# Performance work log

Hardware: AMD Instinct MI355X
Metric: run time of the kernel (lower is better)

Reference implementation:

```python
import jax, jax.numpy as jnp
import numpy as np

B, N, H, HD = 2, 2048, 16, 64
F = H * HD  # feats = 1024
SQRT_D = float(F) ** 0.5  # module uses sqrt(feats), not sqrt(head_dim)
EPS = 1e-5


def layernorm(x, g, b):
    # LayerNorm over last dim (head_dim), shared gamma/beta across heads
    m = jnp.mean(x, axis=-1, keepdims=True)
    v = jnp.mean(jnp.square(x - m), axis=-1, keepdims=True)
    return (x - m) / jnp.sqrt(v + EPS) * g + b


def setup_inputs() -> dict:
    key = jax.random.key(0)
    ks = jax.random.split(key, 14)
    s = 0.02
    return {
        "x": jax.random.normal(ks[0], (B, N, F), dtype=jnp.float32),
        "ln1_g": jnp.ones((HD,), jnp.float32),
        "ln1_b": jnp.zeros((HD,), jnp.float32),
        "ln2_g": jnp.ones((HD,), jnp.float32),
        "ln2_b": jnp.zeros((HD,), jnp.float32),
        # stacked per-head weights: [H, in, out]
        "wq": jax.random.normal(ks[1], (H, HD, HD), jnp.float32) * s,
        "bq": jnp.zeros((H, HD), jnp.float32),
        "wk": jax.random.normal(ks[2], (H, HD, HD), jnp.float32) * s,
        "bk": jnp.zeros((H, HD), jnp.float32),
        "wv": jax.random.normal(ks[3], (H, HD, HD), jnp.float32) * s,
        "bv": jnp.zeros((H, HD), jnp.float32),
        "wo": jax.random.normal(ks[4], (H, HD, HD), jnp.float32) * s,
        "bo": jnp.zeros((H, HD), jnp.float32),
        "w1": jax.random.normal(ks[5], (H, HD, 4 * HD), jnp.float32) * s,
        "b1": jnp.zeros((H, 4 * HD), jnp.float32),
        "w2": jax.random.normal(ks[6], (H, 4 * HD, HD), jnp.float32) * s,
        "b2": jnp.zeros((H, HD), jnp.float32),
        # Method 0 merge Linear(feats, feats): y = x @ wm + bm
        "wm": jax.random.normal(ks[7], (F, F), jnp.float32) * s,
        "bm": jnp.zeros((F,), jnp.float32),
    }


def reference(x, ln1_g, ln1_b, ln2_g, ln2_b, wq, bq, wk, bk, wv, bv, wo, bo,
              w1, b1, w2, b2, wm, bm):
    b, n, f = x.shape
    x4 = x.reshape(b, n, H, HD)  # [b, n, h, hd]

    # --- Multi-head self attention (per-head linears batched over h) ---
    h1 = layernorm(x4, ln1_g, ln1_b)
    q = jnp.einsum("bnhf,hfg->bnhg", h1, wq) + bq
    k = jnp.einsum("bnhf,hfg->bnhg", h1, wk) + bk
    v = jnp.einsum("bnhf,hfg->bnhg", h1, wv) + bv
    qh = jnp.swapaxes(q, 1, 2)  # [b, h, n, hd]
    kh = jnp.swapaxes(k, 1, 2)
    vh = jnp.swapaxes(v, 1, 2)
    score = jax.nn.softmax(jnp.einsum("bhif,bhjf->bhij", qh, kh) / SQRT_D, axis=-1)
    attn = jnp.einsum("bhij,bhjf->bihf", score, vh)  # [b, n, h, hd]
    attn = jnp.einsum("bnhf,hfg->bnhg", attn, wo) + bo
    out = attn + x4

    # --- Per-head FFN (GELU after BOTH linears, as in source; dropout=0) ---
    h2 = layernorm(out, ln2_g, ln2_b)
    t = jax.nn.gelu(jnp.einsum("bnhf,hfg->bnhg", h2, w1) + b1, approximate=False)
    t = jax.nn.gelu(jnp.einsum("bnhg,hgf->bnhf", t, w2) + b2, approximate=False)
    out = t + out

    # --- Method 0 merge ---
    out = out.reshape(b, n, f)
    out = out @ wm + bm
    return out
```

## Files before the change

### kernel.cpp

```cpp
#include <hip/hip_runtime.h>
#include <hip/hip_bf16.h>
#include <math.h>

#define TOKS 4096
#define NSEQ 2048
#define NH 16
#define DH 64
#define FD 1024

typedef __bf16 bf16_t;
typedef bf16_t bf16x4 __attribute__((ext_vector_type(4)));
typedef bf16_t bf16x8 __attribute__((ext_vector_type(8)));
typedef float f32x4 __attribute__((ext_vector_type(4)));

#define GLL16(gsrc, ldst)                                                        \
    __builtin_amdgcn_global_load_lds(                                            \
        (const __attribute__((address_space(1))) void*)(const void*)(gsrc),      \
        (__attribute__((address_space(3))) void*)(void*)(ldst), 16, 0, 0)

__device__ __forceinline__ float geluf(float x) {
    return 0.5f * x * (1.0f + erff(x * 0.70710678118654752f));
}

__device__ __forceinline__ float fexp2(float x) {
    int i = (int)__builtin_fmaf(x, 8388608.0f, 1065063216.0f);
    return __int_as_float(i);
}

__device__ __forceinline__ int lds_sw(int row, int d) {
    return row * 64 + ((((d >> 3) ^ (row & 7)) & 7) << 3) + (d & 7);
}

__device__ __forceinline__ int vperm(int j) {
    return (j & 32) | ((j & 12) << 1) | ((j & 16) >> 2) | (j & 3);
}

__global__ __launch_bounds__(256) void k_prep(
    const float* __restrict__ wm, const float* __restrict__ w1, const float* __restrict__ w2,
    const float* __restrict__ wq, const float* __restrict__ wk,
    const float* __restrict__ wv, const float* __restrict__ wo,
    bf16_t* __restrict__ wt, bf16_t* __restrict__ w1t, bf16_t* __restrict__ w2t,
    bf16_t* __restrict__ wqt, bf16_t* __restrict__ wkt,
    bf16_t* __restrict__ wvt, bf16_t* __restrict__ wot)
{
    __shared__ bf16_t t[64 * 65];
    const int b = blockIdx.x;
    const int tid = threadIdx.x;
    if (b < 256) {
        const int k0 = (b & 15) * 64, n0 = (b >> 4) * 64;
        #pragma unroll
        for (int it = 0; it < 16; it++) {
            int idx = it * 256 + tid;
            int kk = idx >> 6, nn = idx & 63;
            t[nn * 65 + kk] = (bf16_t)wm[(size_t)(k0 + kk) * FD + n0 + nn];
        }
        __syncthreads();
        #pragma unroll
        for (int it = 0; it < 16; it++) {
            int idx = it * 256 + tid;
            int nn = idx >> 6, kk = idx & 63;
            wt[(size_t)(n0 + nn) * FD + k0 + kk] = t[nn * 65 + kk];
        }
    } else if (b < 320) {
        const int lb = b - 256;
        const int h = lb >> 2, n0 = (lb & 3) * 64;
        const float* src = w1 + (size_t)h * 64 * 256;
        #pragma unroll
        for (int it = 0; it < 16; it++) {
            int idx = it * 256 + tid;
            int kk = idx >> 6, nn = idx & 63;
            t[nn * 65 + kk] = (bf16_t)src[kk * 256 + n0 + nn];
        }
        __syncthreads();
        bf16_t* dst = w1t + (size_t)h * 16384;
        #pragma unroll
        for (int it = 0; it < 16; it++) {
            int idx = it * 256 + tid;
            int nn = idx >> 6, kk = idx & 63;
            int row = n0 + nn;
            dst[row * 64 + ((((kk >> 3) ^ (row & 7)) & 7) << 3) + (kk & 7)] = t[nn * 65 + kk];
        }
    } else if (b < 384) {
        const int lb = b - 320;
        const int h = lb >> 2, k0 = (lb & 3) * 64;
        const float* src = w2 + (size_t)h * 256 * 64;
        #pragma unroll
        for (int it = 0; it < 16; it++) {
            int idx = it * 256 + tid;
            int kk = idx >> 6, nn = idx & 63;
            t[nn * 65 + kk] = (bf16_t)src[(k0 + kk) * 64 + nn];
        }
        __syncthreads();
        bf16_t* dst = w2t + (size_t)h * 16384;
        #pragma unroll
        for (int it = 0; it < 16; it++) {
            int idx = it * 256 + tid;
            int nn = idx >> 6, kk = idx & 63;
            int c = k0 + vperm(kk);
            int chunk = c >> 3;
            int chunkp = (chunk & 24) | ((chunk ^ nn) & 7);
            dst[nn * 256 + (chunkp << 3) + (c & 7)] = t[nn * 65 + kk];
        }
    } else {
        const int h = b - 384;
        const float* srcs[4] = {wq + h * 4096, wk + h * 4096, wv + h * 4096, wo + h * 4096};
        bf16_t* dsts[4] = {wqt + h * 4096, wkt + h * 4096, wvt + h * 4096, wot + h * 4096};
        #pragma unroll
        for (int m = 0; m < 4; m++) {
            __syncthreads();
            #pragma unroll
            for (int it = 0; it < 16; it++) {
                int idx = it * 256 + tid;
                int ff = idx >> 6, gg = idx & 63;
                t[gg * 65 + ff] = (bf16_t)srcs[m][ff * 64 + gg];
            }
            __syncthreads();
            #pragma unroll
            for (int it = 0; it < 16; it++) {
                int idx = it * 256 + tid;
                int gg = idx >> 6, ff = idx & 63;
                if (m == 3)
                    dsts[m][gg * 64 + ((((ff >> 3) ^ (gg & 7)) & 7) << 3) + (ff & 7)] =
                        t[gg * 65 + ff];
                else
                    dsts[m][gg * 64 + ff] = t[gg * 65 + ff];
            }
        }
    }
}

__global__ __launch_bounds__(256) void k_ln1_qkv(
    const float* __restrict__ x, const float* __restrict__ g1, const float* __restrict__ be1,
    const bf16_t* __restrict__ wqt, const float* __restrict__ bq,
    const bf16_t* __restrict__ wkt, const float* __restrict__ bk,
    const bf16_t* __restrict__ wvt, const float* __restrict__ bv,
    bf16_t* __restrict__ q, bf16_t* __restrict__ k, bf16_t* __restrict__ vt)
{
    __shared__ __align__(16) bf16_t h1s[64 * 64];
    __shared__ __align__(16) bf16_t vts[64 * 72];
    const int h  = blockIdx.y;
    const int t0 = blockIdx.x * 64;
    const int tid = threadIdx.x;

    {
        const int i = tid >> 2, s = tid & 3;
        const float* xr = x + (size_t)(t0 + i) * FD + h * DH + s * 16;
        float vals[16];
        #pragma unroll
        for (int r = 0; r < 4; r++) {
            float4 tmp = *(const float4*)(xr + r * 4);
            vals[r*4+0]=tmp.x; vals[r*4+1]=tmp.y; vals[r*4+2]=tmp.z; vals[r*4+3]=tmp.w;
        }
        float sm = 0.f;
        #pragma unroll
        for (int r = 0; r < 16; r++) sm += vals[r];
        sm += __shfl_xor(sm, 1); sm += __shfl_xor(sm, 2);
        const float mean = sm * (1.0f / 64.0f);
        float vr = 0.f;
        #pragma unroll
        for (int r = 0; r < 16; r++) { float d = vals[r] - mean; vr += d * d; }
        vr += __shfl_xor(vr, 1); vr += __shfl_xor(vr, 2);
        const float rstd = rsqrtf(vr * (1.0f / 64.0f) + 1e-5f);
        bf16x8 o0, o1;
        #pragma unroll
        for (int r = 0; r < 8; r++) {
            int d0 = s * 16 + r, d1 = s * 16 + 8 + r;
            o0[r] = (bf16_t)((vals[r]     - mean) * rstd * g1[d0] + be1[d0]);
            o1[r] = (bf16_t)((vals[8 + r] - mean) * rstd * g1[d1] + be1[d1]);
        }
        *(bf16x8*)&h1s[i * 64 + (((s * 2 + 0) ^ (i & 7)) << 3)] = o0;
        *(bf16x8*)&h1s[i * 64 + (((s * 2 + 1) ^ (i & 7)) << 3)] = o1;
    }
    __syncthreads();

    const int wid = tid >> 6, lane = tid & 63;
    const int g = lane >> 4, c0 = lane & 15;
    const int arow = wid * 16 + c0;

    bf16x8 af0 = *(const bf16x8*)&h1s[arow * 64 + (((g    ) ^ (arow & 7)) << 3)];
    bf16x8 af1 = *(const bf16x8*)&h1s[arow * 64 + (((4 + g) ^ (arow & 7)) << 3)];

    const bf16_t* wqh = wqt + h * 4096;
    const bf16_t* wkh = wkt + h * 4096;
    const bf16_t* wvh = wvt + h * 4096;
    f32x4 aq[4], ak[4], av[4];
    #pragma unroll
    for (int ni = 0; ni < 4; ni++) {
        aq[ni] = (f32x4){0.f, 0.f, 0.f, 0.f};
        ak[ni] = (f32x4){0.f, 0.f, 0.f, 0.f};
        av[ni] = (f32x4){0.f, 0.f, 0.f, 0.f};
    }
    #pragma unroll
    for (int ni = 0; ni < 4; ni++) {
        const int col = ni * 16 + c0;
        bf16x8 b0, b1;
        b0 = *(const bf16x8*)(wqh + col * 64 + g * 8);
        b1 = *(const bf16x8*)(wqh + col * 64 + g * 8 + 32);
        aq[ni] = __builtin_amdgcn_mfma_f32_16x16x32_bf16(af0, b0, aq[ni], 0, 0, 0);
        aq[ni] = __builtin_amdgcn_mfma_f32_16x16x32_bf16(af1, b1, aq[ni], 0, 0, 0);
        b0 = *(const bf16x8*)(wkh + col * 64 + g * 8);
        b1 = *(const bf16x8*)(wkh + col * 64 + g * 8 + 32);
        ak[ni] = __builtin_amdgcn_mfma_f32_16x16x32_bf16(af0, b0, ak[ni], 0, 0, 0);
        ak[ni] = __builtin_amdgcn_mfma_f32_16x16x32_bf16(af1, b1, ak[ni], 0, 0, 0);
        b0 = *(const bf16x8*)(wvh + col * 64 + g * 8);
        b1 = *(const bf16x8*)(wvh + col * 64 + g * 8 + 32);
        av[ni] = __builtin_amdgcn_mfma_f32_16x16x32_bf16(af0, b0, av[ni], 0, 0, 0);
        av[ni] = __builtin_amdgcn_mfma_f32_16x16x32_bf16(af1, b1, av[ni], 0, 0, 0);
    }

    const int rowb = wid * 16 + g * 4;
    const int b = t0 >> 11, n0 = t0 & (NSEQ - 1);
    const size_t qkbase = ((size_t)(b * NH + h) * NSEQ + n0) * DH;

    #pragma unroll
    for (int ni = 0; ni < 4; ni++) {
        const int col = ni * 16 + c0;
        const float bb = bv[h * 64 + col];
        #pragma unroll
        for (int r = 0; r < 4; r++) {
            int i = rowb + r;
            vts[col * 72 + vperm(i)] = (bf16_t)(av[ni][r] + bb);
        }
    }
    __syncthreads();

    #pragma unroll
    for (int ni = 0; ni < 4; ni++) {
        const int col = ni * 16 + c0;
        const float bb = bq[h * 64 + col];
        #pragma unroll
        for (int r = 0; r < 4; r++)
            h1s[lds_sw(rowb + r, col)] = (bf16_t)((aq[ni][r] + bb) * 0.045084220f);
    }
    __syncthreads();
    {
        const int row = tid >> 2, cp = (tid & 3) * 2;
        *(bf16x8*)(q + qkbase + row * DH + cp * 8) =
            *(const bf16x8*)&h1s[row * 64 + ((cp ^ (row & 7)) << 3)];
        *(bf16x8*)(q + qkbase + row * DH + (cp + 1) * 8) =
            *(const bf16x8*)&h1s[row * 64 + (((cp + 1) ^ (row & 7)) << 3)];
        const int d = tid >> 2, c16 = tid & 3;
        size_t vbase = ((size_t)(b * NH + h) * DH + d) * NSEQ + n0 + c16 * 16;
        *(bf16x8*)(vt + vbase)     = *(const bf16x8*)&vts[d * 72 + c16 * 16];
        *(bf16x8*)(vt + vbase + 8) = *(const bf16x8*)&vts[d * 72 + c16 * 16 + 8];
    }
    __syncthreads();

    #pragma unroll
    for (int ni = 0; ni < 4; ni++) {
        const int col = ni * 16 + c0;
        const float bb = bk[h * 64 + col];
        #pragma unroll
        for (int r = 0; r < 4; r++)
            h1s[lds_sw(rowb + r, col)] = (bf16_t)(ak[ni][r] + bb);
    }
    __syncthreads();
    {
        const int row = tid >> 2, cp = (tid & 3) * 2;
        *(bf16x8*)(k + qkbase + row * DH + cp * 8) =
            *(const bf16x8*)&h1s[row * 64 + ((cp ^ (row & 7)) << 3)];
        *(bf16x8*)(k + qkbase + row * DH + (cp + 1) * 8) =
            *(const bf16x8*)&h1s[row * 64 + (((cp + 1) ^ (row & 7)) << 3)];
    }
}

__global__ __launch_bounds__(256, 4) void k_attn(
    const bf16_t* __restrict__ qg, const bf16_t* __restrict__ kg,
    const bf16_t* __restrict__ vt, bf16_t* __restrict__ attnb)
{
    __shared__ __align__(16) bf16_t Ks[2][4096];
    __shared__ __align__(16) bf16_t Vs[2][4096];

    const int bx = blockIdx.x;
    const int bh = ((bx & 7) << 2) | ((bx >> 3) & 3);
    const int qb = blockIdx.y;
    const int tid = threadIdx.x;
    const int wid = tid >> 6, lane = tid & 63;
    const int g = lane >> 4, c0 = lane & 15;
    const int prow = wid * 16 + c0;

    bf16x8 aqf[2];
    {
        const int qrow = qb * 64 + prow;
        const bf16_t* qp = qg + ((size_t)bh * NSEQ + qrow) * DH + g * 8;
        aqf[0] = *(const bf16x8*)qp;
        aqf[1] = *(const bf16x8*)(qp + 32);
    }
    bf16x8 ones;
    #pragma unroll
    for (int e = 0; e < 8; e++) ones[e] = (bf16_t)1.0f;

    int soff[4][2];
    #pragma unroll
    for (int cb = 0; cb < 4; cb++)
        #pragma unroll
        for (int kb = 0; kb < 2; kb++) {
            int row = cb * 16 + c0;
            soff[cb][kb] = row * 64 + (((g + (kb << 2)) ^ (row & 7)) << 3);
        }

    const bf16_t* kbase = kg + (size_t)bh * NSEQ * DH;
    const bf16_t* vbase = vt + (size_t)bh * DH * NSEQ;
    const int gA = wid * 2, gB = gA + 1;
    const int lcA = gA * 64 + lane, lcB = gB * 64 + lane;
    const int rowA = lcA >> 3, ccA = (lcA & 7) ^ (rowA & 7);
    const int rowB = lcB >> 3, ccB = (lcB & 7) ^ (rowB & 7);
    const bf16_t* kpA = kbase + rowA * DH + ccA * 8;
    const bf16_t* kpB = kbase + rowB * DH + ccB * 8;
    const bf16_t* vpA = vbase + (size_t)rowA * NSEQ + ccA * 8;
    const bf16_t* vpB = vbase + (size_t)rowB * NSEQ + ccB * 8;

    GLL16(kpA, (char*)&Ks[0][0] + (gA << 10));
    GLL16(kpB, (char*)&Ks[0][0] + (gB << 10));
    GLL16(vpA, (char*)&Vs[0][0] + (gA << 10));
    GLL16(vpB, (char*)&Vs[0][0] + (gB << 10));
    kpA += 64 * DH; kpB += 64 * DH; vpA += 64; vpB += 64;

    f32x4 O[4];
    #pragma unroll
    for (int cb = 0; cb < 4; cb++) O[cb] = (f32x4){0.f, 0.f, 0.f, 0.f};
    f32x4 l_acc = (f32x4){0.f, 0.f, 0.f, 0.f};

    auto tile = [&](const bf16_t* Kc, const bf16_t* Vc,
                    bf16_t* Kn, bf16_t* Vn, bool pref) {
        __syncthreads();
        if (pref) {
            GLL16(kpA, (char*)Kn + (gA << 10));
            GLL16(kpB, (char*)Kn + (gB << 10));
            GLL16(vpA, (char*)Vn + (gA << 10));
            GLL16(vpB, (char*)Vn + (gB << 10));
            kpA += 64 * DH; kpB += 64 * DH; vpA += 64; vpB += 64;
        }

        f32x4 S[4];
        #pragma unroll
        for (int cb = 0; cb < 4; cb++) {
            f32x4 acc = (f32x4){0.f, 0.f, 0.f, 0.f};
            acc = __builtin_amdgcn_mfma_f32_16x16x32_bf16(
                *(const bf16x8*)&Kc[soff[cb][0]], aqf[0], acc, 0, 0, 0);
            acc = __builtin_amdgcn_mfma_f32_16x16x32_bf16(
                *(const bf16x8*)&Kc[soff[cb][1]], aqf[1], acc, 0, 0, 0);
            S[cb] = acc;
        }

        bf16x8 pa0, pa1;
        #pragma unroll
        for (int cb = 0; cb < 2; cb++)
            #pragma unroll
            for (int r = 0; r < 4; r++)
                pa0[cb * 4 + r] = (bf16_t)fexp2(S[cb][r]);
        #pragma unroll
        for (int cb = 0; cb < 2; cb++)
            #pragma unroll
            for (int r = 0; r < 4; r++)
                pa1[cb * 4 + r] = (bf16_t)fexp2(S[2 + cb][r]);

        l_acc = __builtin_amdgcn_mfma_f32_16x16x32_bf16(ones, pa0, l_acc, 0, 0, 0);
        l_acc = __builtin_amdgcn_mfma_f32_16x16x32_bf16(ones, pa1, l_acc, 0, 0, 0);

        #pragma unroll
        for (int cb = 0; cb < 4; cb++) {
            f32x4 acc = O[cb];
            acc = __builtin_amdgcn_mfma_f32_16x16x32_bf16(
                *(const bf16x8*)&Vc[soff[cb][0]], pa0, acc, 0, 0, 0);
            acc = __builtin_amdgcn_mfma_f32_16x16x32_bf16(
                *(const bf16x8*)&Vc[soff[cb][1]], pa1, acc, 0, 0, 0);
            O[cb] = acc;
        }
    };

    #pragma unroll 1
    for (int kt2 = 0; kt2 < 16; kt2++) {
        tile(Ks[0], Vs[0], Ks[1], Vs[1], true);
        tile(Ks[1], Vs[1], Ks[0], Vs[0], kt2 < 15);
    }

    __syncthreads();
    const float inv = 1.0f / l_acc[0];
    bf16_t* Tb = Ks[0];
    #pragma unroll
    for (int cb = 0; cb < 4; cb++)
        #pragma unroll
        for (int r = 0; r < 4; r++) {
            int d = cb * 16 + g * 4 + r;
            Tb[lds_sw(prow, d)] = (bf16_t)(O[cb][r] * inv);
        }
    __syncthreads();
    {
        const int row = tid >> 2, cp = (tid & 3) * 2;
        size_t gbase = ((size_t)bh * NSEQ + qb * 64 + row) * DH;
        *(bf16x8*)(attnb + gbase + cp * 8) =
            *(const bf16x8*)&Tb[row * 64 + ((cp ^ (row & 7)) << 3)];
        *(bf16x8*)(attnb + gbase + (cp + 1) * 8) =
            *(const bf16x8*)&Tb[row * 64 + (((cp + 1) ^ (row & 7)) << 3)];
    }
}

__global__ __launch_bounds__(1024) void k_pffn(
    const bf16_t* __restrict__ attnb, const bf16_t* __restrict__ wot,
    const float* __restrict__ bo, const float* __restrict__ x,
    const float* __restrict__ g2, const float* __restrict__ be2,
    const bf16_t* __restrict__ w1t, const float* __restrict__ b1,
    const bf16_t* __restrict__ w2t, const float* __restrict__ b2,
    bf16_t* __restrict__ outp)
{
    __shared__ __align__(16) bf16_t wos[4096];
    __shared__ __align__(16) bf16_t w1s[16384];
    __shared__ __align__(16) bf16_t w2s[16384];
    __shared__ __align__(16) bf16_t h2s[256 * 64];
    const int h  = blockIdx.y;
    const int t0 = blockIdx.x * 256;
    const int tid = threadIdx.x;
    const int wid = tid >> 6, lane = tid & 63;
    const int g = lane >> 4, c0 = lane & 15;
    const int b = t0 >> 11, n0 = t0 & (NSEQ - 1);
    const int tok = t0 + wid * 16 + c0;

    {
        const bf16_t* s0 = wot + h * 4096;
        const bf16_t* s1 = w1t + (size_t)h * 16384;
        const bf16_t* s2 = w2t + (size_t)h * 16384;
        if (wid < 8)
            GLL16(s0 + wid * 512 + lane * 8, (char*)wos + (wid << 10));
        #pragma unroll
        for (int i = 0; i < 2; i++) {
            int grp = wid * 2 + i;
            GLL16(s1 + grp * 512 + lane * 8, (char*)w1s + (grp << 10));
            GLL16(s2 + grp * 512 + lane * 8, (char*)w2s + (grp << 10));
        }
        __syncthreads();
    }

    const bf16_t* ah = attnb + ((size_t)(b * NH + h) * NSEQ + n0) * DH;
    bf16x8 paf0 = *(const bf16x8*)(ah + (wid * 16 + c0) * DH + g * 8);
    bf16x8 paf1 = *(const bf16x8*)(ah + (wid * 16 + c0) * DH + g * 8 + 32);
    float o1[4][4];
    #pragma unroll
    for (int ni = 0; ni < 4; ni++) {
        f32x4 acc = (f32x4){0.f, 0.f, 0.f, 0.f};
        const int orow = ni * 16 + c0;
        bf16x8 b0  = *(const bf16x8*)&wos[orow * 64 + (((g    ) ^ (orow & 7)) << 3)];
        bf16x8 b1f = *(const bf16x8*)&wos[orow * 64 + (((4 + g) ^ (orow & 7)) << 3)];
        acc = __builtin_amdgcn_mfma_f32_16x16x32_bf16(b0, paf0, acc, 0, 0, 0);
        acc = __builtin_amdgcn_mfma_f32_16x16x32_bf16(b1f, paf1, acc, 0, 0, 0);
        const float4 bo4 = *(const float4*)(bo + h * DH + ni * 16 + g * 4);
        const float4 xr4 = *(const float4*)(x + (size_t)tok * FD + h * DH + ni * 16 + g * 4);
        o1[ni][0] = acc[0] + bo4.x + xr4.x;
        o1[ni][1] = acc[1] + bo4.y + xr4.y;
        o1[ni][2] = acc[2] + bo4.z + xr4.z;
        o1[ni][3] = acc[3] + bo4.w + xr4.w;
    }

    float s = 0.f;
    #pragma unroll
    for (int ni = 0; ni < 4; ni++)
        #pragma unroll
        for (int r = 0; r < 4; r++) s += o1[ni][r];
    s += __shfl_xor(s, 16);
    s += __shfl_xor(s, 32);
    const float mean = s * (1.0f / 64.0f);
    float v = 0.f;
    #pragma unroll
    for (int ni = 0; ni < 4; ni++)
        #pragma unroll
        for (int r = 0; r < 4; r++) { float d = o1[ni][r] - mean; v += d * d; }
    v += __shfl_xor(v, 16);
    v += __shfl_xor(v, 32);
    const float rstd = rsqrtf(v * (1.0f / 64.0f) + 1e-5f);

    const int R = wid * 16 + c0;
    #pragma unroll
    for (int ni = 0; ni < 4; ni++) {
        const float4 g24 = *(const float4*)(g2 + ni * 16 + g * 4);
        const float4 be4 = *(const float4*)(be2 + ni * 16 + g * 4);
        bf16x4 hw;
        hw[0] = (bf16_t)((o1[ni][0] - mean) * rstd * g24.x + be4.x);
        hw[1] = (bf16_t)((o1[ni][1] - mean) * rstd * g24.y + be4.y);
        hw[2] = (bf16_t)((o1[ni][2] - mean) * rstd * g24.z + be4.z);
        hw[3] = (bf16_t)((o1[ni][3] - mean) * rstd * g24.w + be4.w);
        int cc = ni * 2 + (g >> 1);
        *(bf16x4*)&h2s[R * 64 + ((cc ^ (R & 7)) << 3) + (g & 1) * 4] = hw;
    }
    bf16x8 af0 = *(const bf16x8*)&h2s[R * 64 + (((g    ) ^ (R & 7)) << 3)];
    bf16x8 af1 = *(const bf16x8*)&h2s[R * 64 + (((4 + g) ^ (R & 7)) << 3)];

    const float* b1h = b1 + h * 256;
    f32x4 acc2[4];
    #pragma unroll
    for (int nt = 0; nt < 4; nt++) acc2[nt] = (f32x4){0.f, 0.f, 0.f, 0.f};

    #pragma unroll
    for (int ub = 0; ub < 4; ub++) {
        f32x4 a4[4];
        #pragma unroll
        for (int j = 0; j < 4; j++) {
            const int wrow = (ub * 4 + j) * 16 + c0;
            bf16x8 bf0 = *(const bf16x8*)&w1s[wrow * 64 + (((g    ) ^ (wrow & 7)) << 3)];
            bf16x8 bf1 = *(const bf16x8*)&w1s[wrow * 64 + (((4 + g) ^ (wrow & 7)) << 3)];
            f32x4 acc = (f32x4){0.f, 0.f, 0.f, 0.f};
            acc = __builtin_amdgcn_mfma_f32_16x16x32_bf16(bf0, af0, acc, 0, 0, 0);
            acc = __builtin_amdgcn_mfma_f32_16x16x32_bf16(bf1, af1, acc, 0, 0, 0);
            a4[j] = acc;
        }
        float4 bb0 = *(const float4*)(b1h + (ub * 4 + 0) * 16 + g * 4);
        float4 bb1 = *(const float4*)(b1h + (ub * 4 + 1) * 16 + g * 4);
        float4 bb2 = *(const float4*)(b1h + (ub * 4 + 2) * 16 + g * 4);
        float4 bb3 = *(const float4*)(b1h + (ub * 4 + 3) * 16 + g * 4);
        bf16x8 p0, p1;
        #pragma unroll
        for (int r = 0; r < 4; r++) {
            p0[r]     = (bf16_t)geluf(a4[0][r] + ((const float*)&bb0)[r]);
            p0[4 + r] = (bf16_t)geluf(a4[1][r] + ((const float*)&bb1)[r]);
            p1[r]     = (bf16_t)geluf(a4[2][r] + ((const float*)&bb2)[r]);
            p1[4 + r] = (bf16_t)geluf(a4[3][r] + ((const float*)&bb3)[r]);
        }
        #pragma unroll
        for (int nt = 0; nt < 4; nt++) {
            const int vrow = nt * 16 + c0;
            bf16x8 bw0 = *(const bf16x8*)&w2s[vrow * 256 +
                            ((ub * 8 + ((g    ) ^ (vrow & 7))) << 3)];
            bf16x8 bw1 = *(const bf16x8*)&w2s[vrow * 256 +
                            ((ub * 8 + ((g + 4) ^ (vrow & 7))) << 3)];
            acc2[nt] = __builtin_amdgcn_mfma_f32_16x16x32_bf16(bw0, p0, acc2[nt], 0, 0, 0);
            acc2[nt] = __builtin_amdgcn_mfma_f32_16x16x32_bf16(bw1, p1, acc2[nt], 0, 0, 0);
        }
    }

    const float* b2h = b2 + h * 64;
    #pragma unroll
    for (int nt = 0; nt < 4; nt++) {
        const float4 b24 = *(const float4*)(b2h + nt * 16 + g * 4);
        bf16x4 ow;
        ow[0] = (bf16_t)(geluf(acc2[nt][0] + b24.x) + o1[nt][0]);
        ow[1] = (bf16_t)(geluf(acc2[nt][1] + b24.y) + o1[nt][1]);
        ow[2] = (bf16_t)(geluf(acc2[nt][2] + b24.z) + o1[nt][2]);
        ow[3] = (bf16_t)(geluf(acc2[nt][3] + b24.w) + o1[nt][3]);
        *(bf16x4*)(outp + (size_t)tok * FD + h * DH + nt * 16 + g * 4) = ow;
    }
}

__global__ __launch_bounds__(256) void k_merge(
    const bf16_t* __restrict__ A, const bf16_t* __restrict__ Wt, const float* __restrict__ bias,
    float* __restrict__ C)
{
    __shared__ __align__(16) bf16_t As[128 * 64];
    __shared__ __align__(16) bf16_t Bs[64 * 64];
    const int n0 = blockIdx.x * 64;
    const int m0 = blockIdx.y * 128;
    const int tid = threadIdx.x;
    const int wid = tid >> 6, lane = tid & 63;
    const int c0 = lane & 15, g = lane >> 4;

    const bf16_t* aS[4]; int aO[4];
    #pragma unroll
    for (int i = 0; i < 4; i++) {
        int grp = wid * 4 + i;
        int lc = grp * 64 + lane;
        int row = lc >> 3, cc = (lc & 7) ^ (row & 7);
        aS[i] = A + (size_t)(m0 + row) * FD + cc * 8;
        aO[i] = grp << 10;
    }
    const bf16_t* bS[2]; int bO[2];
    #pragma unroll
    for (int i = 0; i < 2; i++) {
        int grp = wid * 2 + i;
        int lc = grp * 64 + lane;
        int row = lc >> 3, cc = (lc & 7) ^ (row & 7);
        bS[i] = Wt + (size_t)(n0 + row) * FD + cc * 8;
        bO[i] = grp << 10;
    }

    f32x4 acc[2][4];
    #pragma unroll
    for (int mi = 0; mi < 2; mi++)
        #pragma unroll
        for (int ni = 0; ni < 4; ni++)
            acc[mi][ni] = (f32x4){0.f, 0.f, 0.f, 0.f};

    float bv[4];
    #pragma unroll
    for (int ni = 0; ni < 4; ni++) bv[ni] = bias[n0 + ni * 16 + c0];

    for (int k0 = 0; k0 < FD; k0 += 64) {
        __syncthreads();
        #pragma unroll
        for (int i = 0; i < 4; i++) GLL16(aS[i] + k0, (char*)As + aO[i]);
        #pragma unroll
        for (int i = 0; i < 2; i++) GLL16(bS[i] + k0, (char*)Bs + bO[i]);
        __syncthreads();

        bf16x8 af[2][2];
        #pragma unroll
        for (int mi = 0; mi < 2; mi++)
            #pragma unroll
            for (int kk = 0; kk < 2; kk++) {
                int arow = wid * 32 + mi * 16 + c0;
                int ch = kk * 4 + g;
                af[mi][kk] = *(const bf16x8*)&As[arow * 64 + ((ch ^ (arow & 7)) << 3)];
            }
        bf16x8 bfr[4][2];
        #pragma unroll
        for (int ni = 0; ni < 4; ni++)
            #pragma unroll
            for (int kk = 0; kk < 2; kk++) {
                int brow = ni * 16 + c0;
                int ch = kk * 4 + g;
                bfr[ni][kk] = *(const bf16x8*)&Bs[brow * 64 + ((ch ^ (brow & 7)) << 3)];
            }
        #pragma unroll
        for (int mi = 0; mi < 2; mi++)
            #pragma unroll
            for (int ni = 0; ni < 4; ni++)
                #pragma unroll
                for (int kk = 0; kk < 2; kk++)
                    acc[mi][ni] = __builtin_amdgcn_mfma_f32_16x16x32_bf16(
                        af[mi][kk], bfr[ni][kk], acc[mi][ni], 0, 0, 0);
    }

    #pragma unroll
    for (int mi = 0; mi < 2; mi++)
        #pragma unroll
        for (int r = 0; r < 4; r++) {
            int row = m0 + wid * 32 + mi * 16 + g * 4 + r;
            float* cp = C + (size_t)row * FD + n0;
            #pragma unroll
            for (int ni = 0; ni < 4; ni++)
                cp[ni * 16 + c0] = acc[mi][ni][r] + bv[ni];
        }
}

extern "C" void kernel_launch(void* const* d_in, const int* in_sizes, int n_in,
                              void* d_out, int out_size, void* d_ws, size_t ws_size,
                              hipStream_t stream) {
    const float* x   = (const float*)d_in[0];
    const float* g1  = (const float*)d_in[1];
    const float* be1 = (const float*)d_in[2];
    const float* g2  = (const float*)d_in[3];
    const float* be2 = (const float*)d_in[4];
    const float* wq  = (const float*)d_in[5];
    const float* bq  = (const float*)d_in[6];
    const float* wk  = (const float*)d_in[7];
    const float* bk  = (const float*)d_in[8];
    const float* wv  = (const float*)d_in[9];
    const float* bv  = (const float*)d_in[10];
    const float* wo  = (const float*)d_in[11];
    const float* bo  = (const float*)d_in[12];
    const float* w1  = (const float*)d_in[13];
    const float* b1  = (const float*)d_in[14];
    const float* w2  = (const float*)d_in[15];
    const float* b2  = (const float*)d_in[16];
    const float* wm  = (const float*)d_in[17];
    const float* bm  = (const float*)d_in[18];

    char* wsb = (char*)d_ws;
    bf16_t* qb_   = (bf16_t*)(wsb);
    bf16_t* kb_   = (bf16_t*)(wsb + (size_t)8  * 1048576);
    bf16_t* vtb   = (bf16_t*)(wsb + (size_t)16 * 1048576);
    bf16_t* attnb = (bf16_t*)(wsb + (size_t)24 * 1048576);
    bf16_t* out2  = (bf16_t*)(wsb + (size_t)40 * 1048576);
    bf16_t* wtb   = (bf16_t*)(wsb + (size_t)56 * 1048576);
    bf16_t* w1tb  = (bf16_t*)(wsb + (size_t)58 * 1048576);
    bf16_t* w2tb  = (bf16_t*)(wsb + (size_t)58 * 1048576 + 524288);
    bf16_t* wqtb  = (bf16_t*)(wsb + (size_t)59 * 1048576);
    bf16_t* wktb  = (bf16_t*)(wsb + (size_t)59 * 1048576 + 131072);
    bf16_t* wvtb  = (bf16_t*)(wsb + (size_t)59 * 1048576 + 262144);
    bf16_t* wotb  = (bf16_t*)(wsb + (size_t)59 * 1048576 + 393216);

    k_prep<<<dim3(400), 256, 0, stream>>>(wm, w1, w2, wq, wk, wv, wo,
                                          wtb, w1tb, w2tb, wqtb, wktb, wvtb, wotb);
    k_ln1_qkv<<<dim3(TOKS / 64, NH), 256, 0, stream>>>(x, g1, be1, wqtb, bq, wktb, bk, wvtb, bv,
                                                       qb_, kb_, vtb);
    k_attn<<<dim3(32, NSEQ / 64), 256, 0, stream>>>(qb_, kb_, vtb, attnb);
    k_pffn<<<dim3(TOKS / 256, NH), 1024, 0, stream>>>(attnb, wotb, bo, x, g2, be2,
                                                      w1tb, b1, w2tb, b2, out2);
    k_merge<<<dim3(FD / 64, TOKS / 128), 256, 0, stream>>>(out2, wtb, bm, (float*)d_out);
}
```

Measured before the change: 118.5 us.

## Keep LN2 output in registers via permuted W1 layout; halve pffn block size

The W1 weight prep now permutes the K dimension so that the MFMA accumulator layout of the normalized activations can be fed directly as the B operand. This removes the h2s LDS round-trip and its extra sync-free shared traffic. The pffn kernel also drops from 1024 to 512 threads per block with twice as many blocks and a min-occupancy hint. Residual and bias loads are hoisted ahead of the weight staging so their latency overlaps it. The trade-off is that every block still loads the full per-head weights, so the total weight staging traffic doubles.

```diff
diff --git a/kernel.cpp b/kernel.cpp
--- a/kernel.cpp
+++ b/kernel.cpp
@@ -76,9 +76,12 @@
         #pragma unroll
         for (int it = 0; it < 16; it++) {
             int idx = it * 256 + tid;
-            int nn = idx >> 6, kk = idx & 63;
+            int nn = idx >> 6, kpos = idx & 63;
+            int kb = kpos >> 5, gg = (kpos >> 3) & 3, e = kpos & 7;
+            int f = (kb * 2 + (e >> 2)) * 16 + gg * 4 + (e & 3);
             int row = n0 + nn;
-            dst[row * 64 + ((((kk >> 3) ^ (row & 7)) & 7) << 3) + (kk & 7)] = t[nn * 65 + kk];
+            dst[row * 64 + ((((kpos >> 3) ^ (row & 7)) & 7) << 3) + (kpos & 7)] =
+                t[nn * 65 + f];
         }
     } else if (b < 384) {
         const int lb = b - 320;
@@ -396,7 +399,7 @@
     }
 }
 
-__global__ __launch_bounds__(1024) void k_pffn(
+__global__ __launch_bounds__(512, 4) void k_pffn(
     const bf16_t* __restrict__ attnb, const bf16_t* __restrict__ wot,
     const float* __restrict__ bo, const float* __restrict__ x,
     const float* __restrict__ g2, const float* __restrict__ be2,
@@ -407,33 +410,38 @@
     __shared__ __align__(16) bf16_t wos[4096];
     __shared__ __align__(16) bf16_t w1s[16384];
     __shared__ __align__(16) bf16_t w2s[16384];
-    __shared__ __align__(16) bf16_t h2s[256 * 64];
     const int h  = blockIdx.y;
-    const int t0 = blockIdx.x * 256;
+    const int t0 = blockIdx.x * 128;
     const int tid = threadIdx.x;
     const int wid = tid >> 6, lane = tid & 63;
     const int g = lane >> 4, c0 = lane & 15;
     const int b = t0 >> 11, n0 = t0 & (NSEQ - 1);
     const int tok = t0 + wid * 16 + c0;
 
+    const bf16_t* ah = attnb + ((size_t)(b * NH + h) * NSEQ + n0) * DH;
+    bf16x8 paf0 = *(const bf16x8*)(ah + (wid * 16 + c0) * DH + g * 8);
+    bf16x8 paf1 = *(const bf16x8*)(ah + (wid * 16 + c0) * DH + g * 8 + 32);
+    float4 xr4[4], bo4[4];
+    #pragma unroll
+    for (int ni = 0; ni < 4; ni++) {
+        xr4[ni] = *(const float4*)(x + (size_t)tok * FD + h * DH + ni * 16 + g * 4);
+        bo4[ni] = *(const float4*)(bo + h * DH + ni * 16 + g * 4);
+    }
+
     {
         const bf16_t* s0 = wot + h * 4096;
         const bf16_t* s1 = w1t + (size_t)h * 16384;
         const bf16_t* s2 = w2t + (size_t)h * 16384;
-        if (wid < 8)
-            GLL16(s0 + wid * 512 + lane * 8, (char*)wos + (wid << 10));
-        #pragma unroll
-        for (int i = 0; i < 2; i++) {
-            int grp = wid * 2 + i;
+        GLL16(s0 + wid * 512 + lane * 8, (char*)wos + (wid << 10));
+        #pragma unroll
+        for (int i = 0; i < 4; i++) {
+            int grp = wid * 4 + i;
             GLL16(s1 + grp * 512 + lane * 8, (char*)w1s + (grp << 10));
             GLL16(s2 + grp * 512 + lane * 8, (char*)w2s + (grp << 10));
         }
         __syncthreads();
     }
 
-    const bf16_t* ah = attnb + ((size_t)(b * NH + h) * NSEQ + n0) * DH;
-    bf16x8 paf0 = *(const bf16x8*)(ah + (wid * 16 + c0) * DH + g * 8);
-    bf16x8 paf1 = *(const bf16x8*)(ah + (wid * 16 + c0) * DH + g * 8 + 32);
     float o1[4][4];
     #pragma unroll
     for (int ni = 0; ni < 4; ni++) {
@@ -443,12 +451,10 @@
         bf16x8 b1f = *(const bf16x8*)&wos[orow * 64 + (((4 + g) ^ (orow & 7)) << 3)];
         acc = __builtin_amdgcn_mfma_f32_16x16x32_bf16(b0, paf0, acc, 0, 0, 0);
         acc = __builtin_amdgcn_mfma_f32_16x16x32_bf16(b1f, paf1, acc, 0, 0, 0);
-        const float4 bo4 = *(const float4*)(bo + h * DH + ni * 16 + g * 4);
-        const float4 xr4 = *(const float4*)(x + (size_t)tok * FD + h * DH + ni * 16 + g * 4);
-        o1[ni][0] = acc[0] + bo4.x + xr4.x;
-        o1[ni][1] = acc[1] + bo4.y + xr4.y;
-        o1[ni][2] = acc[2] + bo4.z + xr4.z;
-        o1[ni][3] = acc[3] + bo4.w + xr4.w;
+        o1[ni][0] = acc[0] + bo4[ni].x + xr4[ni].x;
+        o1[ni][1] = acc[1] + bo4[ni].y + xr4[ni].y;
+        o1[ni][2] = acc[2] + bo4[ni].z + xr4[ni].z;
+        o1[ni][3] = acc[3] + bo4[ni].w + xr4[ni].w;
     }
 
     float s = 0.f;
@@ -468,21 +474,19 @@
     v += __shfl_xor(v, 32);
     const float rstd = rsqrtf(v * (1.0f / 64.0f) + 1e-5f);
 
-    const int R = wid * 16 + c0;
+    bf16x8 hb0, hb1;
     #pragma unroll
     for (int ni = 0; ni < 4; ni++) {
         const float4 g24 = *(const float4*)(g2 + ni * 16 + g * 4);
         const float4 be4 = *(const float4*)(be2 + ni * 16 + g * 4);
-        bf16x4 hw;
-        hw[0] = (bf16_t)((o1[ni][0] - mean) * rstd * g24.x + be4.x);
-        hw[1] = (bf16_t)((o1[ni][1] - mean) * rstd * g24.y + be4.y);
-        hw[2] = (bf16_t)((o1[ni][2] - mean) * rstd * g24.z + be4.z);
-        hw[3] = (bf16_t)((o1[ni][3] - mean) * rstd * g24.w + be4.w);
-        int cc = ni * 2 + (g >> 1);
-        *(bf16x4*)&h2s[R * 64 + ((cc ^ (R & 7)) << 3) + (g & 1) * 4] = hw;
-    }
-    bf16x8 af0 = *(const bf16x8*)&h2s[R * 64 + (((g    ) ^ (R & 7)) << 3)];
-    bf16x8 af1 = *(const bf16x8*)&h2s[R * 64 + (((4 + g) ^ (R & 7)) << 3)];
+        #pragma unroll
+        for (int r = 0; r < 4; r++) {
+            float hv = (o1[ni][r] - mean) * rstd * ((const float*)&g24)[r]
+                       + ((const float*)&be4)[r];
+            if (ni < 2) hb0[(ni & 1) * 4 + r] = (bf16_t)hv;
+            else        hb1[(ni & 1) * 4 + r] = (bf16_t)hv;
+        }
+    }
 
     const float* b1h = b1 + h * 256;
     f32x4 acc2[4];
@@ -498,8 +502,8 @@
             bf16x8 bf0 = *(const bf16x8*)&w1s[wrow * 64 + (((g    ) ^ (wrow & 7)) << 3)];
             bf16x8 bf1 = *(const bf16x8*)&w1s[wrow * 64 + (((4 + g) ^ (wrow & 7)) << 3)];
             f32x4 acc = (f32x4){0.f, 0.f, 0.f, 0.f};
-            acc = __builtin_amdgcn_mfma_f32_16x16x32_bf16(bf0, af0, acc, 0, 0, 0);
-            acc = __builtin_amdgcn_mfma_f32_16x16x32_bf16(bf1, af1, acc, 0, 0, 0);
+            acc = __builtin_amdgcn_mfma_f32_16x16x32_bf16(bf0, hb0, acc, 0, 0, 0);
+            acc = __builtin_amdgcn_mfma_f32_16x16x32_bf16(bf1, hb1, acc, 0, 0, 0);
             a4[j] = acc;
         }
         float4 bb0 = *(const float4*)(b1h + (ub * 4 + 0) * 16 + g * 4);
@@ -671,7 +675,7 @@
     k_ln1_qkv<<<dim3(TOKS / 64, NH), 256, 0, stream>>>(x, g1, be1, wqtb, bq, wktb, bk, wvtb, bv,
                                                        qb_, kb_, vtb);
     k_attn<<<dim3(32, NSEQ / 64), 256, 0, stream>>>(qb_, kb_, vtb, attnb);
-    k_pffn<<<dim3(TOKS / 256, NH), 1024, 0, stream>>>(attnb, wotb, bo, x, g2, be2,
-                                                      w1tb, b1, w2tb, b2, out2);
+    k_pffn<<<dim3(TOKS / 128, NH), 512, 0, stream>>>(attnb, wotb, bo, x, g2, be2,
+                                                     w1tb, b1, w2tb, b2, out2);
     k_merge<<<dim3(FD / 64, TOKS / 128), 256, 0, stream>>>(out2, wtb, bm, (float*)d_out);
 }
```

Result: faster. 108.4 us (-8.5%).
